# Kernel optimization log

Measured on AMD Instinct MI355X. Metric: run time of the kernel, lower is better.

Reference implementation:

```python
import jax, jax.numpy as jnp
import numpy as np

SH_C0 = 0.28209479177387814
SH_C1 = 0.4886025119029199
SH_C2 = (1.0925484305920792, -1.0925484305920792, 0.31539156525252005, -1.0925484305920792, 0.5462742152960396)
SH_C3 = (-0.5900435899266435, 2.890611442640554, -0.4570457994644658, 0.3731763325901154, -0.4570457994644658, 1.445305721320277, -0.5900435899266435)

BG = 128  # gaussians per compositing block


def quat_to_rot(q):
    # q: [N,4] normalized quaternion (w,x,y,z) -> [N,3,3]
    w, x, y, z = q[:, 0], q[:, 1], q[:, 2], q[:, 3]
    R = jnp.stack([
        1 - 2 * (y * y + z * z), 2 * (x * y - w * z), 2 * (x * z + w * y),
        2 * (x * y + w * z), 1 - 2 * (x * x + z * z), 2 * (y * z - w * x),
        2 * (x * z - w * y), 2 * (y * z + w * x), 1 - 2 * (x * x + y * y)],
        axis=-1)
    return R.reshape(-1, 3, 3)


def eval_sh(sh, d):
    # sh: [N,16,3] degree-3 SH coeffs; d: [N,3] unit view dirs -> [N,3] rgb
    x, y, z = d[:, 0:1], d[:, 1:2], d[:, 2:3]
    xx, yy, zz = x * x, y * y, z * z
    xy, yz, xz = x * y, y * z, x * z
    res = SH_C0 * sh[:, 0]
    res = res - SH_C1 * y * sh[:, 1] + SH_C1 * z * sh[:, 2] - SH_C1 * x * sh[:, 3]
    res = (res + SH_C2[0] * xy * sh[:, 4] + SH_C2[1] * yz * sh[:, 5]
           + SH_C2[2] * (2 * zz - xx - yy) * sh[:, 6]
           + SH_C2[3] * xz * sh[:, 7] + SH_C2[4] * (xx - yy) * sh[:, 8])
    res = (res + SH_C3[0] * y * (3 * xx - yy) * sh[:, 9] + SH_C3[1] * xy * z * sh[:, 10]
           + SH_C3[2] * y * (4 * zz - xx - yy) * sh[:, 11]
           + SH_C3[3] * z * (2 * zz - 3 * xx - 3 * yy) * sh[:, 12]
           + SH_C3[4] * x * (4 * zz - xx - yy) * sh[:, 13]
           + SH_C3[5] * z * (xx - yy) * sh[:, 14] + SH_C3[6] * x * (xx - 3 * yy) * sh[:, 15])
    return res


def gs_forward(pws, shs, alphas_raw, scales_raw, rots_raw, us, Rcw, tcw, intr, height, width):
    fx, fy, cx, cy = intr[0], intr[1], intr[2], intr[3]
    N = pws.shape[0]
    HW = height * width

    # activations (GSModel.forward)
    alphas = jax.nn.sigmoid(alphas_raw[:, 0])          # [N]
    scales = jnp.exp(scales_raw)                       # [N,3]
    rots = rots_raw / jnp.linalg.norm(rots_raw, axis=1, keepdims=True)

    # gsc.project
    pcs = pws @ Rcw.T + tcw                            # [N,3] camera frame
    depth = pcs[:, 2]
    zs = jnp.where(depth > 0.2, depth, 1.0)            # safe divide for culled pts
    u = jnp.stack([fx * pcs[:, 0] / zs + cx, fy * pcs[:, 1] / zs + cy], axis=-1)
    # the `us` input is a grad-capture dummy; forward value comes from projection
    u = u + us - jax.lax.stop_gradient(us)

    # gsc.computeCov3D: Cov3d = (R S)(R S)^T
    R = quat_to_rot(rots)
    M = R * scales[:, None, :]
    cov3d = M @ jnp.swapaxes(M, 1, 2)                  # [N,3,3]

    # gsc.computeCov2D: cov2d = J W Cov3d W^T J^T + 0.3 I
    tanfx = width / (2.0 * fx)
    tanfy = height / (2.0 * fy)
    tx = jnp.clip(pcs[:, 0] / zs, -1.3 * tanfx, 1.3 * tanfx) * zs
    ty = jnp.clip(pcs[:, 1] / zs, -1.3 * tanfy, 1.3 * tanfy) * zs
    zero = jnp.zeros_like(zs)
    J = jnp.stack([
        fx / zs, zero, -fx * tx / (zs * zs),
        zero, fy / zs, -fy * ty / (zs * zs)], axis=-1).reshape(N, 2, 3)
    T = jnp.einsum('nij,jk->nik', J, Rcw)              # [N,2,3]
    cov2d = jnp.einsum('nij,njk,nlk->nil', T, cov3d, T)
    cov2d = cov2d + 0.3 * jnp.eye(2, dtype=cov2d.dtype)
    a, b, c = cov2d[:, 0, 0], cov2d[:, 0, 1], cov2d[:, 1, 1]
    det = a * c - b * b
    valid = (depth > 0.2) & (det > 0)
    det_s = jnp.where(valid, det, 1.0)

    # gsc.inverseCov2D: conic + screen-space radius (areas)
    cinv = jnp.stack([c / det_s, -b / det_s, a / det_s], axis=-1)  # [N,3]
    mid = 0.5 * (a + c)
    lam = mid + jnp.sqrt(jnp.maximum(mid * mid - det, 0.1))
    radius = jnp.where(valid, jnp.ceil(3.0 * jnp.sqrt(lam)), 0.0)
    areas = jnp.stack([radius, radius], axis=-1)       # [N,2]

    # gsc.sh2Color
    twc = -Rcw.T @ tcw
    dirs = pws - twc
    dirs = dirs / jnp.linalg.norm(dirs, axis=1, keepdims=True)
    colors = jnp.maximum(eval_sh(shs.reshape(N, 16, 3), dirs) + 0.5, 0.0)  # [N,3]

    # gsc.splat: depth-sorted front-to-back alpha compositing over all pixels
    order = jnp.argsort(depth)
    nb = N // BG
    u_s = u[order].reshape(nb, BG, 2)
    cinv_s = cinv[order].reshape(nb, BG, 3)
    al_s = alphas[order].reshape(nb, BG)
    col_s = colors[order].reshape(nb, BG, 3)
    val_s = valid[order].reshape(nb, BG)

    ys, xs = jnp.meshgrid(jnp.arange(height, dtype=jnp.float32),
                          jnp.arange(width, dtype=jnp.float32), indexing='ij')
    px = xs.ravel()
    py = ys.ravel()

    @jax.checkpoint
    def body(carry, blk):
        logT, acc = carry                              # [HW], [3,HW]
        ub, cb, ab, colb, vb = blk
        dx = px[None, :] - ub[:, 0:1]                  # [BG,HW]
        dy = py[None, :] - ub[:, 1:2]
        power = -0.5 * (cb[:, 0:1] * dx * dx + cb[:, 2:3] * dy * dy) - cb[:, 1:2] * dx * dy
        alp = jnp.minimum(0.99, ab[:, None] * jnp.exp(power))
        alp = jnp.where((power <= 0) & (alp >= 1.0 / 255.0) & vb[:, None], alp, 0.0)
        l1m = jnp.log1p(-alp)
        cs = jnp.cumsum(l1m, axis=0)
        logT_i = logT[None, :] + jnp.concatenate(
            [jnp.zeros((1, HW), l1m.dtype), cs[:-1]], axis=0)  # exclusive transmittance
        Ti = jnp.exp(logT_i)
        w = jnp.where(Ti > 1e-4, alp * Ti, 0.0)        # early-termination at tau<1e-4
        acc = acc + jnp.einsum('gp,gc->cp', w, colb)
        return (logT + cs[-1], acc), None

    init = (jnp.zeros(HW, dtype=jnp.float32), jnp.zeros((3, HW), dtype=jnp.float32))
    (_, acc), _ = jax.lax.scan(body, init, (u_s, cinv_s, al_s, col_s, val_s))
    image = acc.reshape(3, height, width)
    return image, areas


def setup_inputs() -> dict:
    key = jax.random.key(0)
    ks = jax.random.split(key, 6)
    N, H, W = 8192, 256, 256
    pws = jax.random.normal(ks[0], (N, 3), jnp.float32) * 2.0 + jnp.array([0.0, 0.0, 6.0])
    shs = jax.random.normal(ks[1], (N, 48), jnp.float32) * 0.3
    alphas_raw = jax.random.normal(ks[2], (N, 1), jnp.float32)
    scales_raw = jax.random.normal(ks[3], (N, 3), jnp.float32) * 0.3 - 3.0
    rots_raw = jax.random.normal(ks[4], (N, 4), jnp.float32)
    us = jnp.zeros((N, 2), jnp.float32)
    Rcw = jnp.eye(3, dtype=jnp.float32)
    tcw = jnp.zeros((3,), jnp.float32)
    intr = jnp.array([400.0, 400.0, 128.0, 128.0], jnp.float32)  # fx, fy, cx, cy
    return {"pws": pws, "shs": shs, "alphas_raw": alphas_raw, "scales_raw": scales_raw,
            "rots_raw": rots_raw, "us": us, "Rcw": Rcw, "tcw": tcw, "intr": intr,
            "height": H, "width": W}


def reference(pws, shs, alphas_raw, scales_raw, rots_raw, us, Rcw, tcw, intr, height, width):
    return gs_forward(pws, shs, alphas_raw, scales_raw, rots_raw, us, Rcw, tcw, intr, height, width)
```

## Files before the change

### kernel.cpp

```cpp
#include <hip/hip_runtime.h>

__global__ __launch_bounds__(256) void k_pre(
    const float* __restrict__ pws, const float* __restrict__ shs,
    const float* __restrict__ alphas_raw, const float* __restrict__ scales_raw,
    const float* __restrict__ rots_raw, const float* __restrict__ Rcw,
    const float* __restrict__ tcw, const float* __restrict__ intr,
    int N, int W, int H, float* __restrict__ areas,
    unsigned long long* __restrict__ keys, unsigned* __restrict__ rank,
    float* __restrict__ P)
{
    int i = blockIdx.x * 256 + threadIdx.x;
    if (i >= N) return;
    rank[i] = 0u;

    float R00=Rcw[0],R01=Rcw[1],R02=Rcw[2];
    float R10=Rcw[3],R11=Rcw[4],R12=Rcw[5];
    float R20=Rcw[6],R21=Rcw[7],R22=Rcw[8];
    float t0=tcw[0],t1=tcw[1],t2=tcw[2];
    float fx=intr[0],fy=intr[1],cx=intr[2],cy=intr[3];

    float pwx=pws[i*3+0], pwy=pws[i*3+1], pwz=pws[i*3+2];
    float pcx = R00*pwx + R01*pwy + R02*pwz + t0;
    float pcy = R10*pwx + R11*pwy + R12*pwz + t1;
    float pcz = R20*pwx + R21*pwy + R22*pwz + t2;
    float depth = pcz;
    float zs = (depth > 0.2f) ? depth : 1.0f;
    float u0 = fx * pcx / zs + cx;
    float u1 = fy * pcy / zs + cy;

    float qw=rots_raw[i*4+0], qx=rots_raw[i*4+1], qy=rots_raw[i*4+2], qz=rots_raw[i*4+3];
    float qn = sqrtf(qw*qw + qx*qx + qy*qy + qz*qz);
    qw/=qn; qx/=qn; qy/=qn; qz/=qn;
    float s0 = expf(scales_raw[i*3+0]);
    float s1 = expf(scales_raw[i*3+1]);
    float s2 = expf(scales_raw[i*3+2]);

    float xx=qx*qx, yy=qy*qy, zq=qz*qz;
    float xy=qx*qy, xz=qx*qz, yz=qy*qz;
    float wx=qw*qx, wy=qw*qy, wz=qw*qz;
    float r00=1.f-2.f*(yy+zq), r01=2.f*(xy-wz),     r02=2.f*(xz+wy);
    float r10=2.f*(xy+wz),     r11=1.f-2.f*(xx+zq), r12=2.f*(yz-wx);
    float r20=2.f*(xz-wy),     r21=2.f*(yz+wx),     r22=1.f-2.f*(xx+yy);

    float m00=r00*s0, m01=r01*s1, m02=r02*s2;
    float m10=r10*s0, m11=r11*s1, m12=r12*s2;
    float m20=r20*s0, m21=r21*s1, m22=r22*s2;
    float V00=m00*m00+m01*m01+m02*m02;
    float V01=m00*m10+m01*m11+m02*m12;
    float V02=m00*m20+m01*m21+m02*m22;
    float V11=m10*m10+m11*m11+m12*m12;
    float V12=m10*m20+m11*m21+m12*m22;
    float V22=m20*m20+m21*m21+m22*m22;

    float tanfx = (float)W / (2.f*fx), tanfy = (float)H / (2.f*fy);
    float limx = 1.3f*tanfx, limy = 1.3f*tanfy;
    float txl = fminf(fmaxf(pcx/zs, -limx), limx) * zs;
    float tyl = fminf(fmaxf(pcy/zs, -limy), limy) * zs;
    float iz = 1.f/zs, iz2 = iz*iz;
    float J00 = fx*iz, J02 = -fx*txl*iz2;
    float J11 = fy*iz, J12 = -fy*tyl*iz2;

    float T00=J00*R00+J02*R20, T01=J00*R01+J02*R21, T02=J00*R02+J02*R22;
    float T10=J11*R10+J12*R20, T11=J11*R11+J12*R21, T12=J11*R12+J12*R22;
    float A0=T00*V00+T01*V01+T02*V02;
    float A1=T00*V01+T01*V11+T02*V12;
    float A2=T00*V02+T01*V12+T02*V22;
    float B0=T10*V00+T11*V01+T12*V02;
    float B1=T10*V01+T11*V11+T12*V12;
    float B2=T10*V02+T11*V12+T12*V22;
    float ca = A0*T00+A1*T01+A2*T02 + 0.3f;
    float cb = A0*T10+A1*T11+A2*T12;
    float cc = B0*T10+B1*T11+B2*T12 + 0.3f;

    float det = ca*cc - cb*cb;
    bool valid = (depth > 0.2f) && (det > 0.f);
    float det_s = valid ? det : 1.f;
    float dinv = 1.f/det_s;
    float ci0 =  cc*dinv, ci1 = -cb*dinv, ci2 = ca*dinv;
    float mid = 0.5f*(ca+cc);
    float lam = mid + sqrtf(fmaxf(mid*mid - det, 0.1f));
    float radius = valid ? ceilf(3.f*sqrtf(lam)) : 0.f;
    areas[2*i+0] = radius;
    areas[2*i+1] = radius;

    float alpha = 1.f/(1.f + expf(-alphas_raw[i]));

    float tw0 = -(R00*t0 + R10*t1 + R20*t2);
    float tw1 = -(R01*t0 + R11*t1 + R21*t2);
    float tw2 = -(R02*t0 + R12*t1 + R22*t2);
    float dx_=pwx-tw0, dy_=pwy-tw1, dz_=pwz-tw2;
    float dn = sqrtf(dx_*dx_+dy_*dy_+dz_*dz_);
    float x=dx_/dn, y=dy_/dn, z=dz_/dn;
    float sxx=x*x, syy=y*y, szz=z*z;
    float sxy=x*y, syz=y*z, sxz=x*z;
    const float* sh = shs + i*48;
    float col[3];
    #pragma unroll
    for (int c = 0; c < 3; ++c) {
        float res = 0.28209479177387814f*sh[0*3+c];
        res += -0.4886025119029199f*y*sh[1*3+c]
             +  0.4886025119029199f*z*sh[2*3+c]
             + -0.4886025119029199f*x*sh[3*3+c];
        res +=  1.0925484305920792f*sxy*sh[4*3+c]
             + -1.0925484305920792f*syz*sh[5*3+c]
             +  0.31539156525252005f*(2.f*szz-sxx-syy)*sh[6*3+c]
             + -1.0925484305920792f*sxz*sh[7*3+c]
             +  0.5462742152960396f*(sxx-syy)*sh[8*3+c];
        res += -0.5900435899266435f*y*(3.f*sxx-syy)*sh[9*3+c]
             +  2.890611442640554f*sxy*z*sh[10*3+c]
             + -0.4570457994644658f*y*(4.f*szz-sxx-syy)*sh[11*3+c]
             +  0.3731763325901154f*z*(2.f*szz-3.f*sxx-3.f*syy)*sh[12*3+c]
             + -0.4570457994644658f*x*(4.f*szz-sxx-syy)*sh[13*3+c]
             +  1.445305721320277f*z*(sxx-syy)*sh[14*3+c]
             + -0.5900435899266435f*x*(sxx-3.f*syy)*sh[15*3+c];
        col[c] = fmaxf(res + 0.5f, 0.f);
    }

    float rc2;
    if (!valid || 255.f*alpha < 0.999f) {
        rc2 = -1.f;
    } else {
        float r2 = 2.f*lam*logf(255.f*alpha);
        float r  = sqrtf(fmaxf(r2, 0.f)) + 1.f;
        rc2 = r*r;
    }

    P[0*N+i]=u0;  P[1*N+i]=u1;  P[2*N+i]=ci0; P[3*N+i]=ci1; P[4*N+i]=ci2;
    P[5*N+i]=alpha; P[6*N+i]=col[0]; P[7*N+i]=col[1]; P[8*N+i]=col[2];
    P[9*N+i]=rc2;

    unsigned ud = __float_as_uint(depth);
    ud = (ud & 0x80000000u) ? ~ud : (ud | 0x80000000u);
    keys[i] = ((unsigned long long)ud << 32) | (unsigned)i;
}

#define JC 512
__global__ __launch_bounds__(256) void k_rank_scatter(
    const unsigned long long* __restrict__ keys, int N,
    unsigned* __restrict__ rank, const float* __restrict__ Pun,
    float4* __restrict__ gA, float4* __restrict__ gB,
    float4* __restrict__ cull)
{
    __shared__ unsigned long long sk[JC];
    const int j0 = blockIdx.y * JC;
    const int nJ = gridDim.y;
    for (int t = threadIdx.x; t < JC; t += 256) {
        int j = j0 + t;
        sk[t] = (j < N) ? keys[j] : ~0ull;
    }
    __syncthreads();

    const int i0 = blockIdx.x * 512 + threadIdx.x;
    const int i1 = i0 + 256;
    unsigned long long my0 = (i0 < N) ? keys[i0] : 0ull;
    unsigned long long my1 = (i1 < N) ? keys[i1] : 0ull;

    int c0 = 0, c1 = 0;
    const ulonglong2* sk2 = (const ulonglong2*)sk;
    #pragma unroll 4
    for (int t = 0; t < JC/2; ++t) {
        ulonglong2 kk = sk2[t];
        c0 += (kk.x < my0) ? 1 : 0;
        c0 += (kk.y < my0) ? 1 : 0;
        c1 += (kk.x < my1) ? 1 : 0;
        c1 += (kk.y < my1) ? 1 : 0;
    }
    if (i0 < N) {
        unsigned old = atomicAdd(&rank[i0], (unsigned)c0 + (1u << 20));
        if ((int)(old >> 20) == nJ - 1) {
            int s = (int)(old & 0xFFFFFu) + c0;
            cull[s] = make_float4(Pun[0*N+i0], Pun[1*N+i0], Pun[9*N+i0], 0.f);
            gA[s]   = make_float4(Pun[2*N+i0], Pun[3*N+i0], Pun[4*N+i0], Pun[5*N+i0]);
            gB[s]   = make_float4(Pun[6*N+i0], Pun[7*N+i0], Pun[8*N+i0], 0.f);
        }
    }
    if (i1 < N) {
        unsigned old = atomicAdd(&rank[i1], (unsigned)c1 + (1u << 20));
        if ((int)(old >> 20) == nJ - 1) {
            int s = (int)(old & 0xFFFFFu) + c1;
            cull[s] = make_float4(Pun[0*N+i1], Pun[1*N+i1], Pun[9*N+i1], 0.f);
            gA[s]   = make_float4(Pun[2*N+i1], Pun[3*N+i1], Pun[4*N+i1], Pun[5*N+i1]);
            gB[s]   = make_float4(Pun[6*N+i1], Pun[7*N+i1], Pun[8*N+i1], 0.f);
        }
    }
}

__global__ __launch_bounds__(64) void k_render(
    const float4* __restrict__ gA, const float4* __restrict__ gB,
    const float4* __restrict__ cull, int N, int W, int H,
    int nTiles, int nseg, float4* __restrict__ segbuf)
{
    const int lane = threadIdx.x;
    const int tilesX = (W + 7) >> 3;
    const int tile = blockIdx.x % nTiles, seg = blockIdx.x / nTiles;
    const int tX = tile % tilesX, tY = tile / tilesX;
    const int ix = (tX << 3) + (lane & 7);
    const int iy = (tY << 3) + (lane >> 3);
    const bool inb = (ix < W) && (iy < H);
    const float pxf = (float)ix, pyf = (float)iy;
    const float tx0 = (float)(tX << 3), ty0 = (float)(tY << 3);
    int tx1i = (tX << 3) + 7; if (tx1i > W-1) tx1i = W-1;
    int ty1i = (tY << 3) + 7; if (ty1i > H-1) ty1i = H-1;
    const float tx1 = (float)tx1i, ty1 = (float)ty1i;

    const int per = (N + nseg - 1) / nseg;
    const int g0 = seg * per;
    const int g1 = min(N, g0 + per);

    float T = inb ? 1.f : 0.f;
    float aR = 0.f, aG = 0.f, aB = 0.f;

    __shared__ float4 sG0[64];
    __shared__ float4 sG1[64];
    __shared__ float  sB2[64];

    for (int base = g0; base < g1; base += 64) {
        int g = base + lane;
        bool ov = false;
        float u0 = 0.f, u1 = 0.f;
        if (g < g1) {
            float4 cu = cull[g];
            u0 = cu.x; u1 = cu.y;
            float cxp = fminf(fmaxf(u0, tx0), tx1);
            float cyp = fminf(fmaxf(u1, ty0), ty1);
            float ddx = u0 - cxp, ddy = u1 - cyp;
            ov = (ddx*ddx + ddy*ddy) <= cu.z;
        }
        unsigned long long m = __ballot(ov);
        int cnt = __popcll(m);
        if (ov) {
            int pos = __popcll(m & ((1ull << lane) - 1ull));
            float4 a4 = gA[g];
            float4 b4 = gB[g];
            sG0[pos] = make_float4(u0, u1, a4.x, a4.y);
            sG1[pos] = make_float4(a4.z, a4.w, b4.x, b4.y);
            sB2[pos] = b4.z;
        }
        for (int e = 0; e < cnt; ++e) {
            float4 e0 = sG0[e];
            float4 e1 = sG1[e];
            float  gb = sB2[e];
            float ddx = pxf - e0.x, ddy = pyf - e0.y;
            float power = -0.5f*(e0.z*ddx*ddx + e1.x*ddy*ddy) - e0.w*ddx*ddy;
            float alp = fminf(0.99f, e1.y * __expf(power));
            alp = (power <= 0.f && alp >= (1.0f/255.0f)) ? alp : 0.f;
            float w = (T > 0.0001f) ? alp * T : 0.f;
            aR = fmaf(w, e1.z, aR);
            aG = fmaf(w, e1.w, aG);
            aB = fmaf(w, gb, aB);
            T = T - T * alp;
        }
        if (__all(T <= 0.0001f)) break;
    }

    if (inb) {
        int pix = iy * W + ix;
        segbuf[(size_t)seg * (size_t)(W*H) + pix] = make_float4(T, aR, aG, aB);
    }
}

__global__ __launch_bounds__(256) void k_combine(
    const float4* __restrict__ segbuf, int HW, int nseg,
    float* __restrict__ out)
{
    int p = blockIdx.x * 256 + threadIdx.x;
    if (p >= HW) return;
    float T = 1.f, r = 0.f, g = 0.f, b = 0.f;
    for (int s = 0; s < nseg; ++s) {
        float4 v = segbuf[(size_t)s * HW + p];
        r = fmaf(T, v.y, r);
        g = fmaf(T, v.z, g);
        b = fmaf(T, v.w, b);
        T *= v.x;
    }
    out[p] = r; out[HW + p] = g; out[2*HW + p] = b;
}

extern "C" void kernel_launch(void* const* d_in, const int* in_sizes, int n_in,
                              void* d_out, int out_size, void* d_ws, size_t ws_size,
                              hipStream_t stream) {
    const float* pws        = (const float*)d_in[0];
    const float* shs        = (const float*)d_in[1];
    const float* alphas_raw = (const float*)d_in[2];
    const float* scales_raw = (const float*)d_in[3];
    const float* rots_raw   = (const float*)d_in[4];
    const float* Rcw        = (const float*)d_in[6];
    const float* tcw        = (const float*)d_in[7];
    const float* intr       = (const float*)d_in[8];

    const int N  = in_sizes[0] / 3;
    const int HW = (out_size - 2 * N) / 3;
    int W = 1; while ((long long)W * W < (long long)HW) ++W;
    const int H = HW / W;

    float* out   = (float*)d_out;
    float* areas = out + 3 * HW;

    char* ws = (char*)d_ws;
    size_t off = 0;
    unsigned long long* keys = (unsigned long long*)(ws + off); off += (size_t)N * 8;
    unsigned* rank = (unsigned*)(ws + off);                     off += (size_t)N * 4;
    off = (off + 15) & ~(size_t)15;
    float* Pun = (float*)(ws + off);                            off += (size_t)10 * N * 4;
    off = (off + 15) & ~(size_t)15;
    float4* cullv = (float4*)(ws + off);                        off += (size_t)N * 16;
    float4* gA = (float4*)(ws + off);                           off += (size_t)N * 16;
    float4* gB = (float4*)(ws + off);                           off += (size_t)N * 16;
    float4* segbuf = (float4*)(ws + off);
    size_t remain = (ws_size > off) ? (ws_size - off) : 0;
    int nseg = 8;
    while (nseg > 1 && (size_t)nseg * (size_t)HW * 16 > remain) nseg >>= 1;

    int gsN = (N + 255) / 256;
    k_pre<<<gsN, 256, 0, stream>>>(pws, shs, alphas_raw, scales_raw, rots_raw,
                                   Rcw, tcw, intr, N, W, H, areas, keys, rank, Pun);
    dim3 rgrid((N + 511) / 512, (N + JC - 1) / JC);
    k_rank_scatter<<<rgrid, 256, 0, stream>>>(keys, N, rank, Pun, gA, gB, cullv);
    int tilesX = (W + 7) / 8, tilesY = (H + 7) / 8;
    int nTiles = tilesX * tilesY;
    k_render<<<nTiles * nseg, 64, 0, stream>>>(gA, gB, cullv, N, W, H,
                                               nTiles, nseg, segbuf);
    k_combine<<<(HW + 255) / 256, 256, 0, stream>>>(segbuf, HW, nseg, out);
}
```

Baseline: 110.3 us.

## Rebalance preprocessing, ranking and render block shapes; vectorize SH and quaternion loads

```diff
diff --git a/kernel.cpp b/kernel.cpp
--- a/kernel.cpp
+++ b/kernel.cpp
@@ -1,6 +1,6 @@
 #include <hip/hip_runtime.h>
 
-__global__ __launch_bounds__(256) void k_pre(
+__global__ __launch_bounds__(64) void k_pre(
     const float* __restrict__ pws, const float* __restrict__ shs,
     const float* __restrict__ alphas_raw, const float* __restrict__ scales_raw,
     const float* __restrict__ rots_raw, const float* __restrict__ Rcw,
@@ -9,7 +9,7 @@
     unsigned long long* __restrict__ keys, unsigned* __restrict__ rank,
     float* __restrict__ P)
 {
-    int i = blockIdx.x * 256 + threadIdx.x;
+    int i = blockIdx.x * 64 + threadIdx.x;
     if (i >= N) return;
     rank[i] = 0u;
 
@@ -28,7 +28,8 @@
     float u0 = fx * pcx / zs + cx;
     float u1 = fy * pcy / zs + cy;
 
-    float qw=rots_raw[i*4+0], qx=rots_raw[i*4+1], qy=rots_raw[i*4+2], qz=rots_raw[i*4+3];
+    float4 q4 = *reinterpret_cast<const float4*>(rots_raw + i*4);
+    float qw=q4.x, qx=q4.y, qy=q4.z, qz=q4.w;
     float qn = sqrtf(qw*qw + qx*qx + qy*qy + qz*qz);
     qw/=qn; qx/=qn; qy/=qn; qz/=qn;
     float s0 = expf(scales_raw[i*3+0]);
@@ -93,26 +94,33 @@
     float x=dx_/dn, y=dy_/dn, z=dz_/dn;
     float sxx=x*x, syy=y*y, szz=z*z;
     float sxy=x*y, syz=y*z, sxz=x*z;
-    const float* sh = shs + i*48;
+
+    float shl[48];
+    const float4* sh4 = reinterpret_cast<const float4*>(shs + i*48);
+    #pragma unroll
+    for (int k = 0; k < 12; ++k) {
+        float4 v = sh4[k];
+        shl[4*k+0]=v.x; shl[4*k+1]=v.y; shl[4*k+2]=v.z; shl[4*k+3]=v.w;
+    }
     float col[3];
     #pragma unroll
     for (int c = 0; c < 3; ++c) {
-        float res = 0.28209479177387814f*sh[0*3+c];
-        res += -0.4886025119029199f*y*sh[1*3+c]
-             +  0.4886025119029199f*z*sh[2*3+c]
-             + -0.4886025119029199f*x*sh[3*3+c];
-        res +=  1.0925484305920792f*sxy*sh[4*3+c]
-             + -1.0925484305920792f*syz*sh[5*3+c]
-             +  0.31539156525252005f*(2.f*szz-sxx-syy)*sh[6*3+c]
-             + -1.0925484305920792f*sxz*sh[7*3+c]
-             +  0.5462742152960396f*(sxx-syy)*sh[8*3+c];
-        res += -0.5900435899266435f*y*(3.f*sxx-syy)*sh[9*3+c]
-             +  2.890611442640554f*sxy*z*sh[10*3+c]
-             + -0.4570457994644658f*y*(4.f*szz-sxx-syy)*sh[11*3+c]
-             +  0.3731763325901154f*z*(2.f*szz-3.f*sxx-3.f*syy)*sh[12*3+c]
-             + -0.4570457994644658f*x*(4.f*szz-sxx-syy)*sh[13*3+c]
-             +  1.445305721320277f*z*(sxx-syy)*sh[14*3+c]
-             + -0.5900435899266435f*x*(sxx-3.f*syy)*sh[15*3+c];
+        float res = 0.28209479177387814f*shl[0*3+c];
+        res += -0.4886025119029199f*y*shl[1*3+c]
+             +  0.4886025119029199f*z*shl[2*3+c]
+             + -0.4886025119029199f*x*shl[3*3+c];
+        res +=  1.0925484305920792f*sxy*shl[4*3+c]
+             + -1.0925484305920792f*syz*shl[5*3+c]
+             +  0.31539156525252005f*(2.f*szz-sxx-syy)*shl[6*3+c]
+             + -1.0925484305920792f*sxz*shl[7*3+c]
+             +  0.5462742152960396f*(sxx-syy)*shl[8*3+c];
+        res += -0.5900435899266435f*y*(3.f*sxx-syy)*shl[9*3+c]
+             +  2.890611442640554f*sxy*z*shl[10*3+c]
+             + -0.4570457994644658f*y*(4.f*szz-sxx-syy)*shl[11*3+c]
+             +  0.3731763325901154f*z*(2.f*szz-3.f*sxx-3.f*syy)*shl[12*3+c]
+             + -0.4570457994644658f*x*(4.f*szz-sxx-syy)*shl[13*3+c]
+             +  1.445305721320277f*z*(sxx-syy)*shl[14*3+c]
+             + -0.5900435899266435f*x*(sxx-3.f*syy)*shl[15*3+c];
         col[c] = fmaxf(res + 0.5f, 0.f);
     }
 
@@ -150,53 +158,44 @@
     }
     __syncthreads();
 
-    const int i0 = blockIdx.x * 512 + threadIdx.x;
-    const int i1 = i0 + 256;
-    unsigned long long my0 = (i0 < N) ? keys[i0] : 0ull;
-    unsigned long long my1 = (i1 < N) ? keys[i1] : 0ull;
-
-    int c0 = 0, c1 = 0;
+    const int i = blockIdx.x * 256 + threadIdx.x;
+    unsigned long long my = (i < N) ? keys[i] : 0ull;
+
+    int c = 0;
     const ulonglong2* sk2 = (const ulonglong2*)sk;
     #pragma unroll 4
     for (int t = 0; t < JC/2; ++t) {
         ulonglong2 kk = sk2[t];
-        c0 += (kk.x < my0) ? 1 : 0;
-        c0 += (kk.y < my0) ? 1 : 0;
-        c1 += (kk.x < my1) ? 1 : 0;
-        c1 += (kk.y < my1) ? 1 : 0;
-    }
-    if (i0 < N) {
-        unsigned old = atomicAdd(&rank[i0], (unsigned)c0 + (1u << 20));
+        c += (kk.x < my) ? 1 : 0;
+        c += (kk.y < my) ? 1 : 0;
+    }
+    if (i < N) {
+        unsigned old = atomicAdd(&rank[i], (unsigned)c + (1u << 20));
         if ((int)(old >> 20) == nJ - 1) {
-            int s = (int)(old & 0xFFFFFu) + c0;
-            cull[s] = make_float4(Pun[0*N+i0], Pun[1*N+i0], Pun[9*N+i0], 0.f);
-            gA[s]   = make_float4(Pun[2*N+i0], Pun[3*N+i0], Pun[4*N+i0], Pun[5*N+i0]);
-            gB[s]   = make_float4(Pun[6*N+i0], Pun[7*N+i0], Pun[8*N+i0], 0.f);
+            int s = (int)(old & 0xFFFFFu) + c;
+            cull[s] = make_float4(Pun[0*N+i], Pun[1*N+i], Pun[9*N+i], 0.f);
+            gA[s]   = make_float4(Pun[2*N+i], Pun[3*N+i], Pun[4*N+i], Pun[5*N+i]);
+            gB[s]   = make_float4(Pun[6*N+i], Pun[7*N+i], Pun[8*N+i], 0.f);
         }
     }
-    if (i1 < N) {
-        unsigned old = atomicAdd(&rank[i1], (unsigned)c1 + (1u << 20));
-        if ((int)(old >> 20) == nJ - 1) {
-            int s = (int)(old & 0xFFFFFu) + c1;
-            cull[s] = make_float4(Pun[0*N+i1], Pun[1*N+i1], Pun[9*N+i1], 0.f);
-            gA[s]   = make_float4(Pun[2*N+i1], Pun[3*N+i1], Pun[4*N+i1], Pun[5*N+i1]);
-            gB[s]   = make_float4(Pun[6*N+i1], Pun[7*N+i1], Pun[8*N+i1], 0.f);
-        }
-    }
-}
-
-__global__ __launch_bounds__(64) void k_render(
+}
+
+__global__ __launch_bounds__(256, 8) void k_render(
     const float4* __restrict__ gA, const float4* __restrict__ gB,
     const float4* __restrict__ cull, int N, int W, int H,
-    int nTiles, int nseg, float4* __restrict__ segbuf)
+    int nSuper, int superX, int tilesX, int tilesY, int nseg,
+    float4* __restrict__ segbuf)
 {
-    const int lane = threadIdx.x;
-    const int tilesX = (W + 7) >> 3;
-    const int tile = blockIdx.x % nTiles, seg = blockIdx.x / nTiles;
-    const int tX = tile % tilesX, tY = tile / tilesX;
+    const int tid  = threadIdx.x;
+    const int wv   = tid >> 6, lane = tid & 63;
+    const int sup  = blockIdx.x % nSuper, seg = blockIdx.x / nSuper;
+    const int sX   = sup % superX, sY = sup / superX;
+    const int tX   = (sX << 1) + (wv & 1);
+    const int tY   = (sY << 1) + (wv >> 1);
+    const bool tOK = (tX < tilesX) && (tY < tilesY);
     const int ix = (tX << 3) + (lane & 7);
     const int iy = (tY << 3) + (lane >> 3);
-    const bool inb = (ix < W) && (iy < H);
+    const bool inb = tOK && (ix < W) && (iy < H);
     const float pxf = (float)ix, pyf = (float)iy;
     const float tx0 = (float)(tX << 3), ty0 = (float)(tY << 3);
     int tx1i = (tX << 3) + 7; if (tx1i > W-1) tx1i = W-1;
@@ -210,47 +209,49 @@
     float T = inb ? 1.f : 0.f;
     float aR = 0.f, aG = 0.f, aB = 0.f;
 
-    __shared__ float4 sG0[64];
-    __shared__ float4 sG1[64];
-    __shared__ float  sB2[64];
-
-    for (int base = g0; base < g1; base += 64) {
-        int g = base + lane;
-        bool ov = false;
-        float u0 = 0.f, u1 = 0.f;
-        if (g < g1) {
-            float4 cu = cull[g];
-            u0 = cu.x; u1 = cu.y;
-            float cxp = fminf(fmaxf(u0, tx0), tx1);
-            float cyp = fminf(fmaxf(u1, ty0), ty1);
-            float ddx = u0 - cxp, ddy = u1 - cyp;
-            ov = (ddx*ddx + ddy*ddy) <= cu.z;
+    __shared__ float4 sG0[4][64];
+    __shared__ float4 sG1[4][64];
+    __shared__ float  sB2[4][64];
+
+    if (tOK) {
+        for (int base = g0; base < g1; base += 64) {
+            int g = base + lane;
+            bool ov = false;
+            float u0 = 0.f, u1 = 0.f;
+            if (g < g1) {
+                float4 cu = cull[g];
+                u0 = cu.x; u1 = cu.y;
+                float cxp = fminf(fmaxf(u0, tx0), tx1);
+                float cyp = fminf(fmaxf(u1, ty0), ty1);
+                float ddx = u0 - cxp, ddy = u1 - cyp;
+                ov = (ddx*ddx + ddy*ddy) <= cu.z;
+            }
+            unsigned long long m = __ballot(ov);
+            int cnt = __popcll(m);
+            if (ov) {
+                int pos = __popcll(m & ((1ull << lane) - 1ull));
+                float4 a4 = gA[g];
+                float4 b4 = gB[g];
+                sG0[wv][pos] = make_float4(u0, u1, a4.x, a4.y);
+                sG1[wv][pos] = make_float4(a4.z, a4.w, b4.x, b4.y);
+                sB2[wv][pos] = b4.z;
+            }
+            for (int e = 0; e < cnt; ++e) {
+                float4 e0 = sG0[wv][e];
+                float4 e1 = sG1[wv][e];
+                float  gb = sB2[wv][e];
+                float ddx = pxf - e0.x, ddy = pyf - e0.y;
+                float power = -0.5f*(e0.z*ddx*ddx + e1.x*ddy*ddy) - e0.w*ddx*ddy;
+                float alp = fminf(0.99f, e1.y * __expf(power));
+                alp = (power <= 0.f && alp >= (1.0f/255.0f)) ? alp : 0.f;
+                float w = (T > 0.0001f) ? alp * T : 0.f;
+                aR = fmaf(w, e1.z, aR);
+                aG = fmaf(w, e1.w, aG);
+                aB = fmaf(w, gb, aB);
+                T = T - T * alp;
+            }
+            if (__all(T <= 0.0001f)) break;
         }
-        unsigned long long m = __ballot(ov);
-        int cnt = __popcll(m);
-        if (ov) {
-            int pos = __popcll(m & ((1ull << lane) - 1ull));
-            float4 a4 = gA[g];
-            float4 b4 = gB[g];
-            sG0[pos] = make_float4(u0, u1, a4.x, a4.y);
-            sG1[pos] = make_float4(a4.z, a4.w, b4.x, b4.y);
-            sB2[pos] = b4.z;
-        }
-        for (int e = 0; e < cnt; ++e) {
-            float4 e0 = sG0[e];
-            float4 e1 = sG1[e];
-            float  gb = sB2[e];
-            float ddx = pxf - e0.x, ddy = pyf - e0.y;
-            float power = -0.5f*(e0.z*ddx*ddx + e1.x*ddy*ddy) - e0.w*ddx*ddy;
-            float alp = fminf(0.99f, e1.y * __expf(power));
-            alp = (power <= 0.f && alp >= (1.0f/255.0f)) ? alp : 0.f;
-            float w = (T > 0.0001f) ? alp * T : 0.f;
-            aR = fmaf(w, e1.z, aR);
-            aG = fmaf(w, e1.w, aG);
-            aB = fmaf(w, gb, aB);
-            T = T - T * alp;
-        }
-        if (__all(T <= 0.0001f)) break;
     }
 
     if (inb) {
@@ -311,14 +312,16 @@
     int nseg = 8;
     while (nseg > 1 && (size_t)nseg * (size_t)HW * 16 > remain) nseg >>= 1;
 
-    int gsN = (N + 255) / 256;
-    k_pre<<<gsN, 256, 0, stream>>>(pws, shs, alphas_raw, scales_raw, rots_raw,
-                                   Rcw, tcw, intr, N, W, H, areas, keys, rank, Pun);
-    dim3 rgrid((N + 511) / 512, (N + JC - 1) / JC);
+    k_pre<<<(N + 63) / 64, 64, 0, stream>>>(pws, shs, alphas_raw, scales_raw,
+                                            rots_raw, Rcw, tcw, intr, N, W, H,
+                                            areas, keys, rank, Pun);
+    dim3 rgrid((N + 255) / 256, (N + JC - 1) / JC);
     k_rank_scatter<<<rgrid, 256, 0, stream>>>(keys, N, rank, Pun, gA, gB, cullv);
     int tilesX = (W + 7) / 8, tilesY = (H + 7) / 8;
-    int nTiles = tilesX * tilesY;
-    k_render<<<nTiles * nseg, 64, 0, stream>>>(gA, gB, cullv, N, W, H,
-                                               nTiles, nseg, segbuf);
+    int superX = (tilesX + 1) / 2, superY = (tilesY + 1) / 2;
+    int nSuper = superX * superY;
+    k_render<<<nSuper * nseg, 256, 0, stream>>>(gA, gB, cullv, N, W, H,
+                                                nSuper, superX, tilesX, tilesY,
+                                                nseg, segbuf);
     k_combine<<<(HW + 255) / 256, 256, 0, stream>>>(segbuf, HW, nseg, out);
 }
```

Result: no change. 108.4 us (-1.7%).
